# Kernel optimization log

Hardware: AMD Instinct MI355X
Metric: run time of the kernel (lower is better)

The kernel has to match this reference:

```python
import jax, jax.numpy as jnp
import numpy as np

N_NODES = 10000
N_EDGES = 640000
N_GRAPHS = 64
D = 128
N_BLOCKS = 2
NEG_SLOPE = 0.01  # F.leaky_relu default


def setup_inputs() -> dict:
    key = jax.random.key(0)
    ks = jax.random.split(key, 9)
    x = jax.random.normal(ks[0], (N_NODES, D), dtype=jnp.float32)
    edge_src = jax.random.randint(ks[1], (N_EDGES,), 0, N_NODES, dtype=jnp.int32)
    edge_dst = jax.random.randint(ks[2], (N_EDGES,), 0, N_NODES, dtype=jnp.int32)
    graph_ids = jnp.sort(jax.random.randint(ks[3], (N_NODES,), 0, N_GRAPHS, dtype=jnp.int32))
    s = 1.414 / np.sqrt(D)  # xavier-normal-ish scale
    Wfc = jax.random.normal(ks[4], (N_BLOCKS, D, D), dtype=jnp.float32) * s
    bfc = jnp.zeros((N_BLOCKS, D), dtype=jnp.float32)
    wl = jax.random.normal(ks[5], (N_BLOCKS, D), dtype=jnp.float32) * s
    wr = jax.random.normal(ks[6], (N_BLOCKS, D), dtype=jnp.float32) * s
    Wres = jax.random.normal(ks[7], (N_BLOCKS, D, D), dtype=jnp.float32) * s
    return {"x": x, "edge_src": edge_src, "edge_dst": edge_dst, "graph_ids": graph_ids,
            "Wfc": Wfc, "bfc": bfc, "wl": wl, "wr": wr, "Wres": Wres}


def _gat_block(x, edge_src, edge_dst, Wfc_b, bfc_b, wl_b, wr_b, Wres_b):
    # node projections: nn.Linear -> x @ W^T + b
    feat = x @ Wfc_b.T + bfc_b                       # [N, D]
    a_self = feat @ wl_b                              # [N] self_a (dst side)
    a_nb = feat @ wr_b                                # [N] attn  (src side)
    # per-edge score: leaky_relu(self_a[dst] + attn[src])
    s = a_self[edge_dst] + a_nb[edge_src]             # [E]
    s = jnp.where(s >= 0, s, NEG_SLOPE * s)
    # segment softmax over incoming edges of each dst node
    m = jax.ops.segment_max(s, edge_dst, num_segments=N_NODES)   # [N]
    e = jnp.exp(s - m[edge_dst])                                  # [E]
    denom = jax.ops.segment_sum(e, edge_dst, num_segments=N_NODES)
    w = e / denom[edge_dst]                                       # [E]
    # attention-weighted neighbor aggregation
    accum = jax.ops.segment_sum(w[:, None] * feat[edge_src], edge_dst,
                                num_segments=N_NODES)             # [N, D]
    # residual (in_size == out_size -> res_fc, no bias), then relu
    out = accum + x @ Wres_b.T
    return jax.nn.relu(out)


def reference(x, edge_src, edge_dst, graph_ids, Wfc, bfc, wl, wr, Wres):
    blocks = [
        _gat_block(x, edge_src, edge_dst, Wfc[b], bfc[b], wl[b], wr[b], Wres[b])
        for b in range(N_BLOCKS)
    ]
    h = jnp.concatenate(blocks, axis=1)               # mode='concat' -> [N, 2*D]
    # dgl.sum_nodes: per-graph sum pooling
    phis = jax.ops.segment_sum(h, graph_ids, num_segments=N_GRAPHS)  # [G, 2*D]
    return h, phis
```

## Files before the change

kernel.cpp:

```cpp
#include <hip/hip_runtime.h>
#include <hip/hip_bf16.h>
#include <math.h>

#define N_NODES 10000
#define N_EDGES 640000
#define N_GRAPHS 64
#define DIM 128
#define NEG_SLOPE 0.01f
#define NB_CSR 128
#define EDGES_PER_BLK (N_EDGES / NB_CSR)


__global__ __launch_bounds__(512) void csr_hist(const int4* __restrict__ edst4,
                                                int* __restrict__ bh) {
    __shared__ int hist[N_NODES];
    const int blk = blockIdx.x;
    const int t = threadIdx.x;
    for (int n = t; n < N_NODES; n += 512) hist[n] = 0;
    __syncthreads();
    const int base4 = blk * (EDGES_PER_BLK / 4);
    for (int i = t; i < EDGES_PER_BLK / 4; i += 512) {
        int4 d = edst4[base4 + i];
        atomicAdd(&hist[d.x], 1);
        atomicAdd(&hist[d.y], 1);
        atomicAdd(&hist[d.z], 1);
        atomicAdd(&hist[d.w], 1);
    }
    __syncthreads();
    int* dst = bh + (size_t)blk * N_NODES;
    for (int n = t; n < N_NODES; n += 512) dst[n] = hist[n];
}

__global__ __launch_bounds__(256) void csr_node_scan(int* __restrict__ bh,
                                                     int* __restrict__ deg) {
    int n = blockIdx.x * 256 + threadIdx.x;
    if (n >= N_NODES) return;
    int running = 0;
    for (int blk = 0; blk < NB_CSR; ++blk) {
        int* p = bh + (size_t)blk * N_NODES + n;
        int v = *p;
        *p = running;
        running += v;
    }
    deg[n] = running;
}

__global__ __launch_bounds__(1024) void scan_deg(const int* __restrict__ deg,
                                                 int* __restrict__ rowptr) {
    __shared__ int sdata[1024];
    const int tid = threadIdx.x;
    const int base = tid * 10;
    int cnt = N_NODES - base;
    if (cnt < 0) cnt = 0;
    if (cnt > 10) cnt = 10;
    int local[10];
    int s = 0;
    for (int i = 0; i < cnt; ++i) { local[i] = s; s += deg[base + i]; }
    sdata[tid] = s;
    __syncthreads();
    for (int off = 1; off < 1024; off <<= 1) {
        int v = 0;
        if (tid >= off) v = sdata[tid - off];
        __syncthreads();
        if (tid >= off) sdata[tid] += v;
        __syncthreads();
    }
    int pre = (tid == 0) ? 0 : sdata[tid - 1];
    for (int i = 0; i < cnt; ++i) rowptr[base + i] = pre + local[i];
    if (tid == 1023) rowptr[N_NODES] = sdata[1023];
}

__global__ __launch_bounds__(512) void csr_scatter(
    const int4* __restrict__ esrc4, const int4* __restrict__ edst4,
    const int* __restrict__ rowptr, const int* __restrict__ bh,
    int* __restrict__ csr_src) {
    __shared__ int cur[N_NODES];
    const int blk = blockIdx.x;
    const int t = threadIdx.x;
    const int* boff = bh + (size_t)blk * N_NODES;
    for (int n = t; n < N_NODES; n += 512) cur[n] = rowptr[n] + boff[n];
    __syncthreads();
    const int base4 = blk * (EDGES_PER_BLK / 4);
    for (int i = t; i < EDGES_PER_BLK / 4; i += 512) {
        int4 s = esrc4[base4 + i];
        int4 d = edst4[base4 + i];
        csr_src[atomicAdd(&cur[d.x], 1)] = s.x;
        csr_src[atomicAdd(&cur[d.y], 1)] = s.y;
        csr_src[atomicAdd(&cur[d.z], 1)] = s.z;
        csr_src[atomicAdd(&cur[d.w], 1)] = s.w;
    }
}

__device__ __forceinline__ unsigned short f2bf(float f) {
    __hip_bfloat16 h = __float2bfloat16(f);
    return *reinterpret_cast<unsigned short*>(&h);
}

__global__ __launch_bounds__(256) void gemm_xwT(
    const float* __restrict__ x, const float* __restrict__ Wfc,
    const float* __restrict__ bfc, const float* __restrict__ Wres,
    float* __restrict__ feat, float* __restrict__ resid,
    unsigned short* __restrict__ feat_b16,
    const float* __restrict__ wl, const float* __restrict__ wr,
    float* __restrict__ a_self, float* __restrict__ a_nb) {
    const int which = blockIdx.z & 1;
    const int b = blockIdx.z >> 1;
    const float* __restrict__ W = (which ? Wres : Wfc) + b * DIM * DIM;
    float* __restrict__ out = (which ? resid : feat) + (size_t)b * N_NODES * DIM;
    const int n0 = blockIdx.x * 64;
    const int j0 = blockIdx.y * 64;

    __shared__ float xs[32][68];
    __shared__ float wsh[32][68];

    const int t = threadIdx.x;
    const int tj = t & 15;
    const int tn = t >> 4;
    const int r = t >> 2;
    const int q = t & 3;

    float acc[4][4];
#pragma unroll
    for (int i = 0; i < 4; ++i)
#pragma unroll
        for (int j = 0; j < 4; ++j) acc[i][j] = 0.f;

    for (int kc = 0; kc < DIM; kc += 32) {
        {
            float v[8];
            int n = n0 + r;
            if (n < N_NODES) {
                const float* p = x + (size_t)n * DIM + kc + q * 8;
                float4 v0 = *reinterpret_cast<const float4*>(p);
                float4 v1 = *reinterpret_cast<const float4*>(p + 4);
                v[0] = v0.x; v[1] = v0.y; v[2] = v0.z; v[3] = v0.w;
                v[4] = v1.x; v[5] = v1.y; v[6] = v1.z; v[7] = v1.w;
            } else {
#pragma unroll
                for (int m = 0; m < 8; ++m) v[m] = 0.f;
            }
#pragma unroll
            for (int m = 0; m < 8; ++m) xs[q * 8 + m][r] = v[m];

            const float* pw = W + (size_t)(j0 + r) * DIM + kc + q * 8;
            float4 w0 = *reinterpret_cast<const float4*>(pw);
            float4 w1 = *reinterpret_cast<const float4*>(pw + 4);
            float wv[8] = {w0.x, w0.y, w0.z, w0.w, w1.x, w1.y, w1.z, w1.w};
#pragma unroll
            for (int m = 0; m < 8; ++m) wsh[q * 8 + m][r] = wv[m];
        }
        __syncthreads();

#pragma unroll
        for (int k = 0; k < 32; ++k) {
            float4 xv = *reinterpret_cast<const float4*>(&xs[k][4 * tn]);
            float4 wv = *reinterpret_cast<const float4*>(&wsh[k][4 * tj]);
            float xa[4] = {xv.x, xv.y, xv.z, xv.w};
            float wa[4] = {wv.x, wv.y, wv.z, wv.w};
#pragma unroll
            for (int i = 0; i < 4; ++i)
#pragma unroll
                for (int j = 0; j < 4; ++j) acc[i][j] += xa[i] * wa[j];
        }
        __syncthreads();
    }

    float wlv[4], wrv[4];
    if (!which) {
#pragma unroll
        for (int k = 0; k < 4; ++k) {
            wlv[k] = wl[b * DIM + j0 + tj * 4 + k];
            wrv[k] = wr[b * DIM + j0 + tj * 4 + k];
        }
    }

#pragma unroll
    for (int i = 0; i < 4; ++i) {
        int n = n0 + tn * 4 + i;
        int j = j0 + tj * 4;
        float4 o;
        o.x = acc[i][0]; o.y = acc[i][1]; o.z = acc[i][2]; o.w = acc[i][3];
        if (!which) {
            const float* bias = bfc + b * DIM + j;
            o.x += bias[0]; o.y += bias[1]; o.z += bias[2]; o.w += bias[3];
        }
        if (n < N_NODES) {
            *reinterpret_cast<float4*>(out + (size_t)n * DIM + j) = o;
            if (!which) {
                ushort4 u;
                u.x = f2bf(o.x); u.y = f2bf(o.y); u.z = f2bf(o.z); u.w = f2bf(o.w);
                *reinterpret_cast<ushort4*>(
                    feat_b16 + ((size_t)b * N_NODES + n) * DIM + j) = u;
            }
        }
        if (!which) {
            float ps = o.x * wlv[0] + o.y * wlv[1] + o.z * wlv[2] + o.w * wlv[3];
            float pr = o.x * wrv[0] + o.y * wrv[1] + o.z * wrv[2] + o.w * wrv[3];
#pragma unroll
            for (int off = 8; off > 0; off >>= 1) {
                ps += __shfl_xor(ps, off, 64);
                pr += __shfl_xor(pr, off, 64);
            }
            if (tj == 0 && n < N_NODES) {
                atomicAdd(&a_self[b * N_NODES + n], ps);
                atomicAdd(&a_nb[b * N_NODES + n], pr);
            }
        }
    }
}

__global__ __launch_bounds__(256) void aggregate(
    const unsigned short* __restrict__ feat_b16, const float* __restrict__ resid,
    const float* __restrict__ a_self, const float* __restrict__ a_nb,
    const int* __restrict__ rowptr, const int* __restrict__ csr_src,
    float* __restrict__ out) {
    const int wave = threadIdx.x >> 6;
    const int lane = threadIdx.x & 63;
    const int n = blockIdx.x * 4 + wave;
    const int b = blockIdx.y;
    const int q = lane >> 4;
    const int l16 = lane & 15;
    const int start = rowptr[n];
    const int end = rowptr[n + 1];

    const float* __restrict__ anb = a_nb + b * N_NODES;
    const uint4* __restrict__ fb =
        reinterpret_cast<const uint4*>(feat_b16 + (size_t)b * N_NODES * DIM);
    const float asl = a_self[b * N_NODES + n];

    float acc[8];
#pragma unroll
    for (int k = 0; k < 8; ++k) acc[k] = 0.f;
    float dpart = 0.f;

    for (int c = start; c < end; c += 64) {
        int j = c + lane;
        float e = 0.f;
        int src = 0;
        if (j < end) {
            src = csr_src[j];
            float s = asl + anb[src];
            s = (s >= 0.f) ? s : NEG_SLOPE * s;
            e = __expf(s);
        }
        dpart += e;
        int cnt = end - c;
        if (cnt > 64) cnt = 64;
        int iters = (cnt + 3) >> 2;

        float w0 = __shfl(e, q, 64);
        int s0 = __shfl(src, q, 64);
        uint4 f0 = fb[(size_t)s0 * 16 + l16];

        for (int i2 = 0; i2 < iters - 1; ++i2) {
            int idx = (i2 + 1) * 4 + q;
            float w1 = __shfl(e, idx, 64);
            int s1 = __shfl(src, idx, 64);
            uint4 f1 = fb[(size_t)s1 * 16 + l16];
#pragma unroll
            for (int k = 0; k < 4; ++k) {
                unsigned int u = (&f0.x)[k];
                float lo = __uint_as_float(u << 16);
                float hi = __uint_as_float(u & 0xffff0000u);
                acc[2 * k]     += w0 * lo;
                acc[2 * k + 1] += w0 * hi;
            }
            w0 = w1; f0 = f1;
        }
#pragma unroll
        for (int k = 0; k < 4; ++k) {
            unsigned int u = (&f0.x)[k];
            float lo = __uint_as_float(u << 16);
            float hi = __uint_as_float(u & 0xffff0000u);
            acc[2 * k]     += w0 * lo;
            acc[2 * k + 1] += w0 * hi;
        }
    }

#pragma unroll
    for (int k = 0; k < 8; ++k) {
        acc[k] += __shfl_xor(acc[k], 16, 64);
        acc[k] += __shfl_xor(acc[k], 32, 64);
    }
    float denom = dpart;
#pragma unroll
    for (int off = 32; off > 0; off >>= 1) denom += __shfl_xor(denom, off, 64);

    if (q == 0) {
        float inv = (end > start) ? 1.f / denom : 0.f;
        const float4* rr = reinterpret_cast<const float4*>(
            resid + ((size_t)b * N_NODES + n) * DIM);
        float4 r0 = rr[l16 * 2];
        float4 r1 = rr[l16 * 2 + 1];
        float4 o0, o1;
        o0.x = fmaxf(acc[0] * inv + r0.x, 0.f);
        o0.y = fmaxf(acc[1] * inv + r0.y, 0.f);
        o0.z = fmaxf(acc[2] * inv + r0.z, 0.f);
        o0.w = fmaxf(acc[3] * inv + r0.w, 0.f);
        o1.x = fmaxf(acc[4] * inv + r1.x, 0.f);
        o1.y = fmaxf(acc[5] * inv + r1.y, 0.f);
        o1.z = fmaxf(acc[6] * inv + r1.z, 0.f);
        o1.w = fmaxf(acc[7] * inv + r1.w, 0.f);
        float4* po = reinterpret_cast<float4*>(out + (size_t)n * (2 * DIM) + b * DIM);
        po[l16 * 2] = o0;
        po[l16 * 2 + 1] = o1;
    }
}

__device__ int lower_bound_dev(const int* __restrict__ a, int n, int key) {
    int lo = 0, hi = n;
    while (lo < hi) {
        int mid = (lo + hi) >> 1;
        if (a[mid] < key) lo = mid + 1;
        else hi = mid;
    }
    return lo;
}

__global__ __launch_bounds__(256) void pool_graphs(
    const float* __restrict__ h, const int* __restrict__ gids,
    float* __restrict__ phis) {
    const int g = blockIdx.x;
    const int chunk = blockIdx.y;
    const int tid = threadIdx.x;
    int lo = lower_bound_dev(gids, N_NODES, g);
    int hi = lower_bound_dev(gids, N_NODES, g + 1);
    float acc = 0.f;
    for (int n = lo + chunk; n < hi; n += 16) acc += h[(size_t)n * (2 * DIM) + tid];
    if (acc != 0.f) atomicAdd(&phis[(size_t)g * (2 * DIM) + tid], acc);
}

extern "C" void kernel_launch(void* const* d_in, const int* in_sizes, int n_in,
                              void* d_out, int out_size, void* d_ws, size_t ws_size,
                              hipStream_t stream) {
    const float* x    = (const float*)d_in[0];
    const int* esrc   = (const int*)d_in[1];
    const int* edst   = (const int*)d_in[2];
    const int* gids   = (const int*)d_in[3];
    const float* Wfc  = (const float*)d_in[4];
    const float* bfc  = (const float*)d_in[5];
    const float* wl   = (const float*)d_in[6];
    const float* wr   = (const float*)d_in[7];
    const float* Wres = (const float*)d_in[8];
    float* out = (float*)d_out;

    char* ws = (char*)d_ws;
    float* feat    = (float*)(ws + 0);
    float* resid   = (float*)(ws + 10240000);
    float* a_self  = (float*)(ws + 20480000);
    float* a_nb    = (float*)(ws + 20560000);
    int*   deg     = (int*)(ws + 20640000);
    int*   rowptr  = (int*)(ws + 20688000);
    int*   csr_src = (int*)(ws + 20784000);
    unsigned short* feat_b16 = (unsigned short*)(ws + 23344000);
    int*   bh      = (int*)(ws + 28464000);

    float* phis = out + (size_t)N_NODES * 2 * DIM;

    hipMemsetAsync(a_self, 0, 4 * N_NODES * sizeof(float), stream);
    hipMemsetAsync(phis, 0, N_GRAPHS * 2 * DIM * sizeof(float), stream);

    csr_hist<<<NB_CSR, 512, 0, stream>>>((const int4*)edst, bh);
    csr_node_scan<<<(N_NODES + 255) / 256, 256, 0, stream>>>(bh, deg);
    scan_deg<<<1, 1024, 0, stream>>>(deg, rowptr);
    csr_scatter<<<NB_CSR, 512, 0, stream>>>(
        (const int4*)esrc, (const int4*)edst, rowptr, bh, csr_src);

    gemm_xwT<<<dim3((N_NODES + 63) / 64, 2, 4), 256, 0, stream>>>(
        x, Wfc, bfc, Wres, feat, resid, feat_b16, wl, wr, a_self, a_nb);
    aggregate<<<dim3(2500, 2), 256, 0, stream>>>(
        feat_b16, resid, a_self, a_nb, rowptr, csr_src, out);
    pool_graphs<<<dim3(N_GRAPHS, 16), 256, 0, stream>>>(out, gids, phis);
}
```

Before: 168.5 us.

## Fuse CSR build into one cooperative kernel and pool graphs inside aggregate

Replaces the four CSR construction kernels with one cooperative-launch kernel that uses grid syncs between the histogram, per-node column scan, block-sum scan and scatter phases. It uses 256 blocks, each scanning 40 nodes in LDS. The separate graph-pooling kernel is removed, and per-graph sums are now atomically accumulated into phis directly from aggregate. The unused fp32 feat write in the GEMM is dropped. This cuts kernel launches and a full pass over h, at the cost of grid-sync overhead, a residency requirement for cooperative launch, and heavy float atomics on phis.

```diff
diff --git a/kernel.cpp b/kernel.cpp
--- a/kernel.cpp
+++ b/kernel.cpp
@@ -1,112 +1,140 @@
 #include <hip/hip_runtime.h>
 #include <hip/hip_bf16.h>
+#include <hip/hip_cooperative_groups.h>
 #include <math.h>
+
+namespace cg = cooperative_groups;
 
 #define N_NODES 10000
 #define N_EDGES 640000
 #define N_GRAPHS 64
 #define DIM 128
 #define NEG_SLOPE 0.01f
-#define NB_CSR 128
-#define EDGES_PER_BLK (N_EDGES / NB_CSR)
-
-
-__global__ __launch_bounds__(512) void csr_hist(const int4* __restrict__ edst4,
-                                                int* __restrict__ bh) {
-    __shared__ int hist[N_NODES];
-    const int blk = blockIdx.x;
-    const int t = threadIdx.x;
-    for (int n = t; n < N_NODES; n += 512) hist[n] = 0;
-    __syncthreads();
-    const int base4 = blk * (EDGES_PER_BLK / 4);
-    for (int i = t; i < EDGES_PER_BLK / 4; i += 512) {
-        int4 d = edst4[base4 + i];
-        atomicAdd(&hist[d.x], 1);
-        atomicAdd(&hist[d.y], 1);
-        atomicAdd(&hist[d.z], 1);
-        atomicAdd(&hist[d.w], 1);
-    }
-    __syncthreads();
-    int* dst = bh + (size_t)blk * N_NODES;
-    for (int n = t; n < N_NODES; n += 512) dst[n] = hist[n];
-}
-
-__global__ __launch_bounds__(256) void csr_node_scan(int* __restrict__ bh,
-                                                     int* __restrict__ deg) {
-    int n = blockIdx.x * 256 + threadIdx.x;
-    if (n >= N_NODES) return;
-    int running = 0;
-    for (int blk = 0; blk < NB_CSR; ++blk) {
-        int* p = bh + (size_t)blk * N_NODES + n;
-        int v = *p;
-        *p = running;
-        running += v;
-    }
-    deg[n] = running;
-}
-
-__global__ __launch_bounds__(1024) void scan_deg(const int* __restrict__ deg,
-                                                 int* __restrict__ rowptr) {
-    __shared__ int sdata[1024];
-    const int tid = threadIdx.x;
-    const int base = tid * 10;
-    int cnt = N_NODES - base;
-    if (cnt < 0) cnt = 0;
-    if (cnt > 10) cnt = 10;
-    int local[10];
-    int s = 0;
-    for (int i = 0; i < cnt; ++i) { local[i] = s; s += deg[base + i]; }
-    sdata[tid] = s;
-    __syncthreads();
-    for (int off = 1; off < 1024; off <<= 1) {
-        int v = 0;
-        if (tid >= off) v = sdata[tid - off];
-        __syncthreads();
-        if (tid >= off) sdata[tid] += v;
-        __syncthreads();
-    }
-    int pre = (tid == 0) ? 0 : sdata[tid - 1];
-    for (int i = 0; i < cnt; ++i) rowptr[base + i] = pre + local[i];
-    if (tid == 1023) rowptr[N_NODES] = sdata[1023];
-}
-
-__global__ __launch_bounds__(512) void csr_scatter(
-    const int4* __restrict__ esrc4, const int4* __restrict__ edst4,
-    const int* __restrict__ rowptr, const int* __restrict__ bh,
-    int* __restrict__ csr_src) {
-    __shared__ int cur[N_NODES];
-    const int blk = blockIdx.x;
-    const int t = threadIdx.x;
-    const int* boff = bh + (size_t)blk * N_NODES;
-    for (int n = t; n < N_NODES; n += 512) cur[n] = rowptr[n] + boff[n];
-    __syncthreads();
-    const int base4 = blk * (EDGES_PER_BLK / 4);
-    for (int i = t; i < EDGES_PER_BLK / 4; i += 512) {
-        int4 s = esrc4[base4 + i];
-        int4 d = edst4[base4 + i];
-        csr_src[atomicAdd(&cur[d.x], 1)] = s.x;
-        csr_src[atomicAdd(&cur[d.y], 1)] = s.y;
-        csr_src[atomicAdd(&cur[d.z], 1)] = s.z;
-        csr_src[atomicAdd(&cur[d.w], 1)] = s.w;
-    }
-}
+#define NBC 256
+#define EPB (N_EDGES / NBC)
+#define NPB 40
+
 
 __device__ __forceinline__ unsigned short f2bf(float f) {
     __hip_bfloat16 h = __float2bfloat16(f);
     return *reinterpret_cast<unsigned short*>(&h);
 }
 
+__global__ __launch_bounds__(512) void csr_build(
+    const int4* __restrict__ esrc4, const int4* __restrict__ edst4,
+    int* __restrict__ bh, int* __restrict__ blocksum,
+    int* __restrict__ rowptr, int* __restrict__ csr_src) {
+    cg::grid_group grid = cg::this_grid();
+    __shared__ int lds[NBC * NPB];
+    __shared__ int part[NPB][9];
+    __shared__ int colbase[NPB + 1];
+    const int blk = blockIdx.x;
+    const int t = threadIdx.x;
+    const int base4 = blk * (EPB / 4);
+
+    for (int n = t; n < N_NODES; n += 512) lds[n] = 0;
+    __syncthreads();
+    for (int i = t; i < EPB / 4; i += 512) {
+        int4 d = edst4[base4 + i];
+        atomicAdd(&lds[d.x], 1);
+        atomicAdd(&lds[d.y], 1);
+        atomicAdd(&lds[d.z], 1);
+        atomicAdd(&lds[d.w], 1);
+    }
+    __syncthreads();
+    for (int n = t; n < N_NODES; n += 512) bh[(size_t)blk * N_NODES + n] = lds[n];
+    grid.sync();
+
+    const int nb0 = blk * NPB;
+    for (int idx = t; idx < NBC * NPB; idx += 512) {
+        int r = idx / NPB, j = idx - r * NPB;
+        int n = nb0 + j;
+        lds[idx] = (n < N_NODES) ? bh[(size_t)r * N_NODES + n] : 0;
+    }
+    __syncthreads();
+    const int cj = t >> 3, cs = t & 7;
+    if (t < 320) {
+        int sum = 0;
+#pragma unroll 8
+        for (int r = cs * 32; r < cs * 32 + 32; ++r) sum += lds[r * NPB + cj];
+        part[cj][cs] = sum;
+    }
+    __syncthreads();
+    if (t < NPB) {
+        int run = 0;
+#pragma unroll
+        for (int s2 = 0; s2 < 8; ++s2) { int v = part[t][s2]; part[t][s2] = run; run += v; }
+        colbase[t] = run;
+    }
+    __syncthreads();
+    if (t < 320) {
+        int run = part[cj][cs];
+#pragma unroll 8
+        for (int r = cs * 32; r < cs * 32 + 32; ++r) {
+            int v = lds[r * NPB + cj];
+            lds[r * NPB + cj] = run;
+            run += v;
+        }
+    }
+    __syncthreads();
+    for (int idx = t; idx < NBC * NPB; idx += 512) {
+        int r = idx / NPB, j = idx - r * NPB;
+        int n = nb0 + j;
+        if (n < N_NODES) bh[(size_t)r * N_NODES + n] = lds[idx];
+    }
+    if (t == 0) {
+        int run = 0;
+#pragma unroll
+        for (int j = 0; j < NPB; ++j) { int v = colbase[j]; colbase[j] = run; run += v; }
+        colbase[NPB] = run;
+        blocksum[blk] = run;
+    }
+    grid.sync();
+
+    if (t < 64) {
+        int4 v = reinterpret_cast<const int4*>(blocksum)[t];
+        int lsum = v.x + v.y + v.z + v.w;
+        int inc = lsum;
+#pragma unroll
+        for (int off = 1; off < 64; off <<= 1) {
+            int o = __shfl_up(inc, off, 64);
+            if (t >= off) inc += o;
+        }
+        int excl = inc - lsum;
+        lds[4 * t]     = excl;
+        lds[4 * t + 1] = excl + v.x;
+        lds[4 * t + 2] = excl + v.x + v.y;
+        lds[4 * t + 3] = excl + v.x + v.y + v.z;
+        if (t == 63) lds[256] = inc;
+    }
+    __syncthreads();
+    if (blk == 0 && t == 0) rowptr[N_NODES] = lds[256];
+    if (t < NPB && nb0 + t < N_NODES) rowptr[nb0 + t] = lds[blk] + colbase[t];
+    grid.sync();
+
+    for (int n = t; n < N_NODES; n += 512)
+        lds[n] = rowptr[n] + bh[(size_t)blk * N_NODES + n];
+    __syncthreads();
+    for (int i = t; i < EPB / 4; i += 512) {
+        int4 s = esrc4[base4 + i];
+        int4 d = edst4[base4 + i];
+        csr_src[atomicAdd(&lds[d.x], 1)] = s.x;
+        csr_src[atomicAdd(&lds[d.y], 1)] = s.y;
+        csr_src[atomicAdd(&lds[d.z], 1)] = s.z;
+        csr_src[atomicAdd(&lds[d.w], 1)] = s.w;
+    }
+}
+
 __global__ __launch_bounds__(256) void gemm_xwT(
     const float* __restrict__ x, const float* __restrict__ Wfc,
     const float* __restrict__ bfc, const float* __restrict__ Wres,
-    float* __restrict__ feat, float* __restrict__ resid,
-    unsigned short* __restrict__ feat_b16,
+    float* __restrict__ resid, unsigned short* __restrict__ feat_b16,
     const float* __restrict__ wl, const float* __restrict__ wr,
     float* __restrict__ a_self, float* __restrict__ a_nb) {
     const int which = blockIdx.z & 1;
     const int b = blockIdx.z >> 1;
     const float* __restrict__ W = (which ? Wres : Wfc) + b * DIM * DIM;
-    float* __restrict__ out = (which ? resid : feat) + (size_t)b * N_NODES * DIM;
+    float* __restrict__ outw = resid + (size_t)b * N_NODES * DIM;
     const int n0 = blockIdx.x * 64;
     const int j0 = blockIdx.y * 64;
 
@@ -185,8 +213,9 @@
             o.x += bias[0]; o.y += bias[1]; o.z += bias[2]; o.w += bias[3];
         }
         if (n < N_NODES) {
-            *reinterpret_cast<float4*>(out + (size_t)n * DIM + j) = o;
-            if (!which) {
+            if (which) {
+                *reinterpret_cast<float4*>(outw + (size_t)n * DIM + j) = o;
+            } else {
                 ushort4 u;
                 u.x = f2bf(o.x); u.y = f2bf(o.y); u.z = f2bf(o.z); u.w = f2bf(o.w);
                 *reinterpret_cast<ushort4*>(
@@ -213,7 +242,8 @@
     const unsigned short* __restrict__ feat_b16, const float* __restrict__ resid,
     const float* __restrict__ a_self, const float* __restrict__ a_nb,
     const int* __restrict__ rowptr, const int* __restrict__ csr_src,
-    float* __restrict__ out) {
+    const int* __restrict__ gids, float* __restrict__ out,
+    float* __restrict__ phis) {
     const int wave = threadIdx.x >> 6;
     const int lane = threadIdx.x & 63;
     const int n = blockIdx.x * 4 + wave;
@@ -304,30 +334,14 @@
         float4* po = reinterpret_cast<float4*>(out + (size_t)n * (2 * DIM) + b * DIM);
         po[l16 * 2] = o0;
         po[l16 * 2 + 1] = o1;
-    }
-}
-
-__device__ int lower_bound_dev(const int* __restrict__ a, int n, int key) {
-    int lo = 0, hi = n;
-    while (lo < hi) {
-        int mid = (lo + hi) >> 1;
-        if (a[mid] < key) lo = mid + 1;
-        else hi = mid;
-    }
-    return lo;
-}
-
-__global__ __launch_bounds__(256) void pool_graphs(
-    const float* __restrict__ h, const int* __restrict__ gids,
-    float* __restrict__ phis) {
-    const int g = blockIdx.x;
-    const int chunk = blockIdx.y;
-    const int tid = threadIdx.x;
-    int lo = lower_bound_dev(gids, N_NODES, g);
-    int hi = lower_bound_dev(gids, N_NODES, g + 1);
-    float acc = 0.f;
-    for (int n = lo + chunk; n < hi; n += 16) acc += h[(size_t)n * (2 * DIM) + tid];
-    if (acc != 0.f) atomicAdd(&phis[(size_t)g * (2 * DIM) + tid], acc);
+
+        const int g = gids[n];
+        float* ph = phis + (size_t)g * (2 * DIM) + b * DIM + l16 * 8;
+        atomicAdd(ph + 0, o0.x); atomicAdd(ph + 1, o0.y);
+        atomicAdd(ph + 2, o0.z); atomicAdd(ph + 3, o0.w);
+        atomicAdd(ph + 4, o1.x); atomicAdd(ph + 5, o1.y);
+        atomicAdd(ph + 6, o1.z); atomicAdd(ph + 7, o1.w);
+    }
 }
 
 extern "C" void kernel_launch(void* const* d_in, const int* in_sizes, int n_in,
@@ -345,30 +359,30 @@
     float* out = (float*)d_out;
 
     char* ws = (char*)d_ws;
-    float* feat    = (float*)(ws + 0);
-    float* resid   = (float*)(ws + 10240000);
-    float* a_self  = (float*)(ws + 20480000);
-    float* a_nb    = (float*)(ws + 20560000);
-    int*   deg     = (int*)(ws + 20640000);
-    int*   rowptr  = (int*)(ws + 20688000);
-    int*   csr_src = (int*)(ws + 20784000);
+    int*   bh       = (int*)(ws + 0);
+    float* resid    = (float*)(ws + 10240000);
+    float* a_self   = (float*)(ws + 20480000);
+    float* a_nb     = (float*)(ws + 20560000);
+    int*   blocksum = (int*)(ws + 20640000);
+    int*   rowptr   = (int*)(ws + 20688000);
+    int*   csr_src  = (int*)(ws + 20784000);
     unsigned short* feat_b16 = (unsigned short*)(ws + 23344000);
-    int*   bh      = (int*)(ws + 28464000);
 
     float* phis = out + (size_t)N_NODES * 2 * DIM;
 
     hipMemsetAsync(a_self, 0, 4 * N_NODES * sizeof(float), stream);
     hipMemsetAsync(phis, 0, N_GRAPHS * 2 * DIM * sizeof(float), stream);
 
-    csr_hist<<<NB_CSR, 512, 0, stream>>>((const int4*)edst, bh);
-    csr_node_scan<<<(N_NODES + 255) / 256, 256, 0, stream>>>(bh, deg);
-    scan_deg<<<1, 1024, 0, stream>>>(deg, rowptr);
-    csr_scatter<<<NB_CSR, 512, 0, stream>>>(
-        (const int4*)esrc, (const int4*)edst, rowptr, bh, csr_src);
+    const int4* esrc4 = (const int4*)esrc;
+    const int4* edst4 = (const int4*)edst;
+    void* cargs[] = {(void*)&esrc4, (void*)&edst4, (void*)&bh,
+                     (void*)&blocksum, (void*)&rowptr, (void*)&csr_src};
+    hipLaunchCooperativeKernel((const void*)csr_build, dim3(NBC), dim3(512),
+                               cargs, 0, stream);
 
     gemm_xwT<<<dim3((N_NODES + 63) / 64, 2, 4), 256, 0, stream>>>(
-        x, Wfc, bfc, Wres, feat, resid, feat_b16, wl, wr, a_self, a_nb);
+        x, Wfc, bfc, Wres, resid, feat_b16, wl, wr, a_self, a_nb);
+
     aggregate<<<dim3(2500, 2), 256, 0, stream>>>(
-        feat_b16, resid, a_self, a_nb, rowptr, csr_src, out);
-    pool_graphs<<<dim3(N_GRAPHS, 16), 256, 0, stream>>>(out, gids, phis);
-}
+        feat_b16, resid, a_self, a_nb, rowptr, csr_src, gids, out, phis);
+}
```

Result: slower. 403.3 us (+139.3%).
